# Kernel optimization log

Measured on AMD Instinct MI355X. Metric: run time of the kernel, lower is better.

## Reference

```python
import jax, jax.numpy as jnp
import numpy as np

DECAY = 0.25  # global `decay` in source
EPS = 1e-5    # nn.BatchNorm2d default eps


def quant(x):
    # MultiSpike1: round(clamp(x, 0, 1))
    return jnp.round(jnp.clip(x, 0.0, 1.0))


def lif(x):
    # mem_update: sequential LIF recurrence over time dim T.
    # step0: mem = x[0] (init mem_old=0, spike=0 reproduces it exactly).
    def step(carry, xi):
        mem_old, spike = carry
        mem = (mem_old - jax.lax.stop_gradient(spike) * 0.5) * DECAY + xi
        s = quant(mem)
        return (mem, s), s

    z = jnp.zeros_like(x[0])
    _, out = jax.lax.scan(step, (z, z), x)
    return out  # [T,B,C,H,W]


def setup_inputs() -> dict:
    key = jax.random.key(0)
    k1, k2 = jax.random.split(key, 2)
    T, B, C1, C2, H, W = 4, 8, 64, 128, 128, 128
    x = jax.random.normal(k1, (T, B, C1, H, W), dtype=jnp.float32)
    # Conv2d(c1=64, c2=128, k=3, s=1, pad=1, bias=False)
    conv_w = jax.random.normal(k2, (C2, C1, 3, 3), dtype=jnp.float32) * 0.05
    gamma = jnp.ones((C2,), dtype=jnp.float32)
    beta = jnp.zeros((C2,), dtype=jnp.float32)
    return {"x": x, "conv_w": conv_w, "gamma": gamma, "beta": beta}


def reference(x, conv_w, gamma, beta):
    T, B, C, H, W = x.shape
    C2 = conv_w.shape[0]
    s = lif(x).reshape(T * B, C, H, W)  # flatten(0,1)
    y = jax.lax.conv_general_dilated(
        s, conv_w, window_strides=(1, 1), padding=((1, 1), (1, 1)),
        dimension_numbers=("NCHW", "OIHW", "NCHW"))
    # BatchNorm2d in training mode: batch statistics over (N,H,W), biased var
    mean = y.mean(axis=(0, 2, 3), keepdims=True)
    var = ((y - mean) ** 2).mean(axis=(0, 2, 3), keepdims=True)
    y = (y - mean) * jax.lax.rsqrt(var + EPS)
    y = y * gamma[None, :, None, None] + beta[None, :, None, None]
    return y.reshape(T, B, C2, H, W)
```

## Files before the change

kernel.cpp:

```cpp
#include <hip/hip_runtime.h>

typedef __bf16 bf16x8 __attribute__((ext_vector_type(8)));
typedef float f32x4 __attribute__((ext_vector_type(4)));

#define TBCHW_PLANE 8388608
#define NPIX 524288.0f
#define NBLK 4096
#define SLOT_B 16640

__global__ __launch_bounds__(256) void prep_w(const float* __restrict__ w,
                                              __bf16* __restrict__ wf) {
    int o = blockIdx.x * 256 + threadIdx.x;
    if (o >= 73728) return;
    int j = o & 7;
    int lane = (o >> 3) & 63;
    int mtile = (o >> 9) & 7;
    int kc = o >> 12;
    int k = kc * 32 + (lane >> 4) * 8 + j;
    int c2 = mtile * 16 + (lane & 15);
    int tap = k >> 6, c = k & 63;
    int kh = tap / 3, kw = tap % 3;
    wf[o] = (__bf16)w[((c2 * 64 + c) * 3 + kh) * 3 + kw];
}

__device__ __forceinline__ float lif_step(float& mem, float sp, float xv) {
    mem = (mem - sp * 0.5f) * 0.25f + xv;
    return rintf(fminf(fmaxf(mem, 0.0f), 1.0f));
}

__global__ __launch_bounds__(256) void lif_kernel(const float* __restrict__ x,
                                                  __bf16* __restrict__ s) {
    __shared__ __bf16 lds[2 * 128 * 72];
    int b = blockIdx.x >> 7, h = blockIdx.x & 127;
    int tid = threadIdx.x;

    float4 mem[8], sp[8];
#pragma unroll
    for (int i = 0; i < 8; ++i) { mem[i] = make_float4(0,0,0,0); sp[i] = make_float4(0,0,0,0); }

    for (int half = 0; half < 2; ++half) {
        if (half) __syncthreads();
#pragma unroll
        for (int t2 = 0; t2 < 2; ++t2) {
            int t = half * 2 + t2;
#pragma unroll
            for (int i = 0; i < 8; ++i) {
                int p = tid + 256 * i;
                int c = p >> 5, w0 = (p & 31) * 4;
                const float4 xv = *(const float4*)(x + (size_t)t * TBCHW_PLANE +
                                   (((size_t)b * 64 + c) * 128 + h) * 128 + w0);
                float s0 = lif_step(mem[i].x, sp[i].x, xv.x);
                float s1 = lif_step(mem[i].y, sp[i].y, xv.y);
                float s2 = lif_step(mem[i].z, sp[i].z, xv.z);
                float s3 = lif_step(mem[i].w, sp[i].w, xv.w);
                sp[i] = make_float4(s0, s1, s2, s3);
                int cs = c ^ ((p & 7) << 3);
                __bf16* dst = &lds[(t2 * 128 + w0) * 72 + cs];
                dst[0] = (__bf16)s0; dst[72] = (__bf16)s1;
                dst[144] = (__bf16)s2; dst[216] = (__bf16)s3;
            }
        }
        __syncthreads();
#pragma unroll
        for (int i = 0; i < 8; ++i) {
            int u = tid + 256 * i;
            int t2 = u >> 10, inner = u & 1023;
            int w = inner >> 3, c8 = inner & 7;
            int c8s = c8 ^ ((w >> 2) & 7);
            bf16x8 v = *(const bf16x8*)&lds[(t2 * 128 + w) * 72 + c8s * 8];
            int n = (half * 2 + t2) * 8 + b;
            *(bf16x8*)(s + (((size_t)n * 128 + h) * 128 + w) * 64 + c8 * 8) = v;
        }
    }
}

__global__ __launch_bounds__(256, 3) void conv_kernel(const __bf16* __restrict__ s,
                                                      const __bf16* __restrict__ wf,
                                                      float* __restrict__ out,
                                                      float* __restrict__ part) {
    __shared__ __align__(16) char sb3[3 * SLOT_B];
    const int p = blockIdx.x;
    const int bid = (p & 7) * 512 + (p >> 3);
    const int n = bid >> 7, h = bid & 127;
    const int tid = threadIdx.x;

#pragma unroll
    for (int r = 0; r < 3; ++r) {
        int hh = h + r - 1;
        char* slot = sb3 + r * SLOT_B;
        if (hh >= 0 && hh < 128) {
            const char* src = (const char*)s + (((size_t)n * 128 + hh) << 14);
#pragma unroll
            for (int i = 0; i < 4; ++i) {
                int g = i * 256 + tid;
                int w = g >> 3;
                int sg = (w << 7) + (((g & 7) ^ ((w + 1) & 7)) << 4);
                __builtin_amdgcn_global_load_lds(
                    (const __attribute__((address_space(1))) unsigned int*)(src + sg),
                    (__attribute__((address_space(3))) unsigned int*)(slot + 128 + g * 16),
                    16, 0, 0);
            }
        } else {
            f32x4 z = {0.f, 0.f, 0.f, 0.f};
#pragma unroll
            for (int i = 0; i < 4; ++i)
                *(f32x4*)(slot + 128 + (i * 256 + tid) * 16) = z;
        }
    }
    if (tid < 48) {
        int r = tid / 16, q16 = tid % 16;
        int col = q16 & 1, g8 = q16 >> 1;
        f32x4 z = {0.f, 0.f, 0.f, 0.f};
        *(f32x4*)(sb3 + r * SLOT_B + (col ? 129 * 128 : 0) + g8 * 16) = z;
    }

    const int lane = tid & 63, wave = tid >> 6;
    const int wm = wave >> 1, wn = wave & 1;
    const int lm = lane & 15, q = lane >> 4;
    const int wbyte = (wn * 64 + lm) * 128;

    bf16x8 aC[4], aN[4];
#pragma unroll
    for (int i = 0; i < 4; ++i)
        aC[i] = *(const bf16x8*)(wf + (((size_t)wm * 4 + i) * 64 + lane) * 8);

    __syncthreads();

    f32x4 acc[4][4];
#pragma unroll
    for (int i = 0; i < 4; ++i)
#pragma unroll
        for (int j = 0; j < 4; ++j)
#pragma unroll
            for (int e = 0; e < 4; ++e) acc[i][j][e] = 0.0f;

#pragma unroll
    for (int kc = 0; kc < 18; ++kc) {
        const int tap = kc >> 1;
        const int kh = tap / 3, kw = tap - kh * 3;
        const int c8b = (kc & 1) * 4;
        const char* rb = sb3 + kh * SLOT_B;
        const int off = kw * 128 + (((c8b + q) ^ ((lm + kw) & 7)) << 4);
        if (kc < 17) {
#pragma unroll
            for (int i = 0; i < 4; ++i)
                aN[i] = *(const bf16x8*)(wf + (((size_t)(kc + 1) * 8 + wm * 4 + i) * 64 + lane) * 8);
        }
        bf16x8 bb[4];
#pragma unroll
        for (int j = 0; j < 4; ++j)
            bb[j] = *(const bf16x8*)(rb + wbyte + j * 2048 + off);
#pragma unroll
        for (int i = 0; i < 4; ++i)
#pragma unroll
            for (int j = 0; j < 4; ++j)
                acc[i][j] = __builtin_amdgcn_mfma_f32_16x16x32_bf16(aC[i], bb[j], acc[i][j], 0, 0, 0);
#pragma unroll
        for (int i = 0; i < 4; ++i) aC[i] = aN[i];
    }

    __syncthreads();
    float2* P = (float2*)sb3;

#pragma unroll
    for (int i = 0; i < 4; ++i) {
#pragma unroll
        for (int r = 0; r < 4; ++r) {
            int c2 = wm * 64 + i * 16 + q * 4 + r;
            size_t ob = ((size_t)(n * 128 + c2) * 128 + h) * 128 + wn * 64 + lm;
            float sum = 0.0f, ssq = 0.0f;
#pragma unroll
            for (int j = 0; j < 4; ++j) {
                float v = acc[i][j][r];
                out[ob + j * 16] = v;
                sum += v; ssq += v * v;
            }
#pragma unroll
            for (int d = 8; d > 0; d >>= 1) {
                sum += __shfl_down(sum, d);
                ssq += __shfl_down(ssq, d);
            }
            if (lm == 0) {
                P[wave * 64 + i * 16 + q * 4 + r] = make_float2(sum, ssq);
            }
        }
    }
    __syncthreads();
    {
        int stat = tid >> 7, c2x = tid & 127;
        int wp = c2x >> 6, idx = c2x & 63;
        float2 a2 = P[(wp * 2) * 64 + idx];
        float2 b2 = P[(wp * 2 + 1) * 64 + idx];
        float val = stat ? (a2.y + b2.y) : (a2.x + b2.x);
        part[(size_t)tid * NBLK + bid] = val;
    }
}

__global__ __launch_bounds__(256) void reduce_stats(const float* __restrict__ part,
                                                    const float* __restrict__ gamma,
                                                    const float* __restrict__ beta,
                                                    float* __restrict__ ss) {
    int c = blockIdx.x;
    int tid = threadIdx.x;
    const float* ps = part + (size_t)c * NBLK;
    const float* pq = part + (size_t)(128 + c) * NBLK;
    float sum = 0.0f, ssq = 0.0f;
    for (int i = tid; i < NBLK; i += 256) { sum += ps[i]; ssq += pq[i]; }
#pragma unroll
    for (int d = 32; d > 0; d >>= 1) {
        sum += __shfl_down(sum, d);
        ssq += __shfl_down(ssq, d);
    }
    __shared__ float2 wred[4];
    if ((tid & 63) == 0) wred[tid >> 6] = make_float2(sum, ssq);
    __syncthreads();
    if (tid == 0) {
        float S = 0.0f, Q = 0.0f;
#pragma unroll
        for (int w2 = 0; w2 < 4; ++w2) { S += wred[w2].x; Q += wred[w2].y; }
        const float inv = 1.0f / NPIX;
        float mean = S * inv;
        float var = Q * inv - mean * mean;
        float sc = gamma[c] * rsqrtf(var + 1e-5f);
        ss[c] = sc;
        ss[128 + c] = beta[c] - mean * sc;
    }
}

__global__ __launch_bounds__(256) void bn_apply(float* __restrict__ out,
                                                const float* __restrict__ ss) {
    const size_t stride = (size_t)2048 * 256;
    for (size_t i4 = (size_t)blockIdx.x * 256 + threadIdx.x; i4 < 16777216; i4 += stride) {
        int c2 = (int)((i4 >> 12) & 127);
        float sc = ss[c2], sh = ss[128 + c2];
        float4* p = (float4*)out + i4;
        float4 v = *p;
        v.x = v.x * sc + sh; v.y = v.y * sc + sh;
        v.z = v.z * sc + sh; v.w = v.w * sc + sh;
        *p = v;
    }
}

extern "C" void kernel_launch(void* const* d_in, const int* in_sizes, int n_in,
                              void* d_out, int out_size, void* d_ws, size_t ws_size,
                              hipStream_t stream) {
    const float* x     = (const float*)d_in[0];
    const float* cw    = (const float*)d_in[1];
    const float* gamma = (const float*)d_in[2];
    const float* beta  = (const float*)d_in[3];
    float* out = (float*)d_out;

    char* ws = (char*)d_ws;
    __bf16* s     = (__bf16*)ws;
    __bf16* wfrag = (__bf16*)(ws + 67108864);
    float*  part  = (float*)(ws + 67108864 + 147456);
    float*  ss    = part + 256 * NBLK;

    prep_w      <<<288,   256, 0, stream>>>(cw, wfrag);
    lif_kernel  <<<1024,  256, 0, stream>>>(x, s);
    conv_kernel <<<NBLK,  256, 0, stream>>>(s, wfrag, out, part);
    reduce_stats<<<128,   256, 0, stream>>>(part, gamma, beta, ss);
    bn_apply    <<<2048,  256, 0, stream>>>(out, ss);
}
```

Baseline: 538.5 us.

## Store conv output as bf16 intermediate and split stats reduction into two stages

The conv kernel now writes its pre-normalization output as bf16 to a workspace buffer instead of fp32 into the final output. bn_apply reads that bf16 buffer and writes normalized fp32. This replaces the fp32 read-modify-write pass and cuts conv store and BN read traffic. The per-block statistics layout is transposed to block-major, and the single 128-block reduction is replaced by a coalesced two-stage reduction. Rounding pre-BN values to bf16 adds precision error to the final output, and the extra launch adds a little overhead.

```diff
diff --git a/kernel.cpp b/kernel.cpp
--- a/kernel.cpp
+++ b/kernel.cpp
@@ -76,7 +76,7 @@
 
 __global__ __launch_bounds__(256, 3) void conv_kernel(const __bf16* __restrict__ s,
                                                       const __bf16* __restrict__ wf,
-                                                      float* __restrict__ out,
+                                                      __bf16* __restrict__ y,
                                                       float* __restrict__ part) {
     __shared__ __align__(16) char sb3[3 * SLOT_B];
     const int p = blockIdx.x;
@@ -172,7 +172,7 @@
 #pragma unroll
             for (int j = 0; j < 4; ++j) {
                 float v = acc[i][j][r];
-                out[ob + j * 16] = v;
+                y[ob + j * 16] = (__bf16)v;
                 sum += v; ssq += v * v;
             }
 #pragma unroll
@@ -187,57 +187,63 @@
     }
     __syncthreads();
     {
-        int stat = tid >> 7, c2x = tid & 127;
+        int c2x = tid & 127;
         int wp = c2x >> 6, idx = c2x & 63;
         float2 a2 = P[(wp * 2) * 64 + idx];
         float2 b2 = P[(wp * 2 + 1) * 64 + idx];
-        float val = stat ? (a2.y + b2.y) : (a2.x + b2.x);
-        part[(size_t)tid * NBLK + bid] = val;
-    }
-}
-
-__global__ __launch_bounds__(256) void reduce_stats(const float* __restrict__ part,
-                                                    const float* __restrict__ gamma,
-                                                    const float* __restrict__ beta,
-                                                    float* __restrict__ ss) {
-    int c = blockIdx.x;
+        float val = (tid >> 7) ? (a2.y + b2.y) : (a2.x + b2.x);
+        part[(size_t)bid * 256 + tid] = val;
+    }
+}
+
+__global__ __launch_bounds__(256) void reduce_stage1(const float* __restrict__ part,
+                                                     float* __restrict__ part2) {
     int tid = threadIdx.x;
-    const float* ps = part + (size_t)c * NBLK;
-    const float* pq = part + (size_t)(128 + c) * NBLK;
-    float sum = 0.0f, ssq = 0.0f;
-    for (int i = tid; i < NBLK; i += 256) { sum += ps[i]; ssq += pq[i]; }
-#pragma unroll
-    for (int d = 32; d > 0; d >>= 1) {
-        sum += __shfl_down(sum, d);
-        ssq += __shfl_down(ssq, d);
-    }
-    __shared__ float2 wred[4];
-    if ((tid & 63) == 0) wred[tid >> 6] = make_float2(sum, ssq);
-    __syncthreads();
-    if (tid == 0) {
-        float S = 0.0f, Q = 0.0f;
-#pragma unroll
-        for (int w2 = 0; w2 < 4; ++w2) { S += wred[w2].x; Q += wred[w2].y; }
+    float acc = 0.0f;
+    const float* base = part + (size_t)blockIdx.x * 64 * 256;
+#pragma unroll 8
+    for (int r = 0; r < 64; ++r) acc += base[r * 256 + tid];
+    part2[blockIdx.x * 256 + tid] = acc;
+}
+
+__global__ __launch_bounds__(256) void reduce_stage2(const float* __restrict__ part2,
+                                                     const float* __restrict__ gamma,
+                                                     const float* __restrict__ beta,
+                                                     float* __restrict__ ss) {
+    int tid = threadIdx.x;
+    float tot = 0.0f;
+#pragma unroll 8
+    for (int b = 0; b < 64; ++b) tot += part2[b * 256 + tid];
+    __shared__ float T[256];
+    T[tid] = tot;
+    __syncthreads();
+    if (tid < 128) {
         const float inv = 1.0f / NPIX;
-        float mean = S * inv;
-        float var = Q * inv - mean * mean;
-        float sc = gamma[c] * rsqrtf(var + 1e-5f);
-        ss[c] = sc;
-        ss[128 + c] = beta[c] - mean * sc;
-    }
-}
-
-__global__ __launch_bounds__(256) void bn_apply(float* __restrict__ out,
+        float mean = T[tid] * inv;
+        float var = T[128 + tid] * inv - mean * mean;
+        float sc = gamma[tid] * rsqrtf(var + 1e-5f);
+        ss[tid] = sc;
+        ss[128 + tid] = beta[tid] - mean * sc;
+    }
+}
+
+__global__ __launch_bounds__(256) void bn_apply(const __bf16* __restrict__ y,
+                                                float* __restrict__ out,
                                                 const float* __restrict__ ss) {
     const size_t stride = (size_t)2048 * 256;
-    for (size_t i4 = (size_t)blockIdx.x * 256 + threadIdx.x; i4 < 16777216; i4 += stride) {
-        int c2 = (int)((i4 >> 12) & 127);
+    for (size_t i8 = (size_t)blockIdx.x * 256 + threadIdx.x; i8 < 8388608; i8 += stride) {
+        int c2 = (int)((i8 >> 11) & 127);
         float sc = ss[c2], sh = ss[128 + c2];
-        float4* p = (float4*)out + i4;
-        float4 v = *p;
-        v.x = v.x * sc + sh; v.y = v.y * sc + sh;
-        v.z = v.z * sc + sh; v.w = v.w * sc + sh;
-        *p = v;
+        bf16x8 v = *(const bf16x8*)(y + i8 * 8);
+        f32x4 o0, o1;
+#pragma unroll
+        for (int e = 0; e < 4; ++e) {
+            o0[e] = (float)v[e] * sc + sh;
+            o1[e] = (float)v[4 + e] * sc + sh;
+        }
+        f32x4* dst = (f32x4*)out + i8 * 2;
+        dst[0] = o0;
+        dst[1] = o1;
     }
 }
 
@@ -252,13 +258,16 @@
 
     char* ws = (char*)d_ws;
     __bf16* s     = (__bf16*)ws;
-    __bf16* wfrag = (__bf16*)(ws + 67108864);
-    float*  part  = (float*)(ws + 67108864 + 147456);
-    float*  ss    = part + 256 * NBLK;
-
-    prep_w      <<<288,   256, 0, stream>>>(cw, wfrag);
-    lif_kernel  <<<1024,  256, 0, stream>>>(x, s);
-    conv_kernel <<<NBLK,  256, 0, stream>>>(s, wfrag, out, part);
-    reduce_stats<<<128,   256, 0, stream>>>(part, gamma, beta, ss);
-    bn_apply    <<<2048,  256, 0, stream>>>(out, ss);
-}
+    __bf16* y     = (__bf16*)(ws + 67108864);
+    __bf16* wfrag = (__bf16*)(ws + 201326592);
+    float*  part  = (float*)(ws + 201474048);
+    float*  part2 = (float*)(ws + 205668352);
+    float*  ss    = (float*)(ws + 205733888);
+
+    prep_w       <<<288,   256, 0, stream>>>(cw, wfrag);
+    lif_kernel   <<<1024,  256, 0, stream>>>(x, s);
+    conv_kernel  <<<NBLK,  256, 0, stream>>>(s, wfrag, y, part);
+    reduce_stage1<<<64,    256, 0, stream>>>(part, part2);
+    reduce_stage2<<<1,     256, 0, stream>>>(part2, gamma, beta, ss);
+    bn_apply     <<<2048,  256, 0, stream>>>(y, out, ss);
+}
```

Result: faster. 519.3 us (-3.6%).
